# Kernel optimization log

Measured on AMD Instinct MI355X. Metric: run time of the kernel, lower is better.

## Reference

```python
import jax, jax.numpy as jnp
import numpy as np

NPOINT, RADIUS, NSAMPLE = 1024, 0.2, 32


def setup_inputs() -> dict:
    key = jax.random.key(0)
    ks = jax.random.split(key, 8)
    B, N, C = 16, 4096, 64
    xyz = jax.random.uniform(ks[0], (B, N, 3), jnp.float32)          # points in unit cube
    features = jax.random.normal(ks[1], (B, N, C), jnp.float32)
    W1 = jax.random.normal(ks[2], (64, C + 3), jnp.float32) * 0.05   # Conv2d(67,64,1)
    b1 = jnp.zeros((64,), jnp.float32)
    W2 = jax.random.normal(ks[3], (64, 64), jnp.float32) * 0.05      # Conv2d(64,64,1)
    b2 = jnp.zeros((64,), jnp.float32)
    W3 = jax.random.normal(ks[4], (128, 64), jnp.float32) * 0.05     # Conv2d(64,128,1)
    b3 = jnp.zeros((128,), jnp.float32)
    return {"xyz": xyz, "features": features, "W1": W1, "b1": b1,
            "W2": W2, "b2": b2, "W3": W3, "b3": b3}


def farthest_point_sampling(xyz, npoint):
    # Sequential iterative selection (classic FPS) via lax.scan.
    B, N, _ = xyz.shape
    def step(carry, _):
        dist, far = carry                                            # [B,N], [B]
        centroid = jnp.take_along_axis(xyz, far[:, None, None], axis=1)  # [B,1,3]
        d = jnp.sum((xyz - centroid) ** 2, axis=-1)                  # [B,N]
        dist = jnp.minimum(dist, d)
        nxt = jnp.argmax(dist, axis=-1).astype(jnp.int32)
        return (dist, nxt), far
    init = (jnp.full((B, N), 1e10, xyz.dtype), jnp.zeros((B,), jnp.int32))
    _, idx = jax.lax.scan(step, init, None, length=npoint)
    return idx.T                                                     # [B, npoint]


def ball_query(xyz, new_xyz, radius, nsample):
    B, N, _ = xyz.shape
    S = new_xyz.shape[1]
    sqd = jnp.sum((new_xyz[:, :, None, :] - xyz[:, None, :, :]) ** 2, axis=-1)  # [B,S,N]
    idx = jnp.broadcast_to(jnp.arange(N, dtype=jnp.int32), (B, S, N))
    idx = jnp.where(sqd > radius * radius, N, idx)
    idx = jnp.sort(idx, axis=-1)[:, :, :nsample]                     # first nsample in-ball
    first = idx[:, :, :1]
    return jnp.where(idx == N, first, idx)                           # pad with first hit


def _gather(points, idx):
    # points [B,N,C], idx [B,S,K] -> [B,S,K,C]
    B = points.shape[0]
    return points[jnp.arange(B)[:, None, None], idx]


def reference(xyz, features, W1, b1, W2, b2, W3, b3):
    fps_idx = farthest_point_sampling(xyz, NPOINT)                   # [B,S]
    new_xyz = jnp.take_along_axis(xyz, fps_idx[..., None], axis=1)   # [B,S,3]
    idx = ball_query(xyz, new_xyz, RADIUS, NSAMPLE)                  # [B,S,K]
    grouped_xyz = _gather(xyz, idx) - new_xyz[:, :, None, :]         # [B,S,K,3]
    grouped = jnp.concatenate([grouped_xyz, _gather(features, idx)], axis=-1)  # [B,S,K,3+C]
    x = jnp.transpose(grouped, (0, 3, 2, 1))                          # [B, 3+C, K, S]
    # 1x1 Conv2d stack (no activations in the original Sequential)
    x = jnp.einsum('oc,bckn->bokn', W1, x) + b1[None, :, None, None]
    x = jnp.einsum('oc,bckn->bokn', W2, x) + b2[None, :, None, None]
    x = jnp.einsum('oc,bckn->bokn', W3, x) + b3[None, :, None, None]
    new_features = jnp.max(x, axis=2)                                 # max over nsample -> [B,128,S]
    return new_xyz, new_features, fps_idx
```

## Files before the change

kernel.cpp:

```cpp
#include <hip/hip_runtime.h>
#include <cstdint>
#include <cstddef>

#define B_      16
#define N_      4096
#define CFEAT_  64
#define NPOINT_ 1024
#define NSAMPLE_ 32
#define CIN_    67
#define KPAD_   96
#define COUT_   128
#define R2_     0.04f

typedef float f32x2 __attribute__((ext_vector_type(2)));
typedef float f32x4 __attribute__((ext_vector_type(4)));
typedef short bf16x8 __attribute__((ext_vector_type(8)));

__device__ __forceinline__ f32x2 pk_sub(f32x2 a, f32x2 b) {
  f32x2 d;
  asm("v_pk_add_f32 %0, %1, %2 neg_lo:[0,1] neg_hi:[0,1]" : "=v"(d) : "v"(a), "v"(b));
  return d;
}
__device__ __forceinline__ f32x2 pk_mul(f32x2 a, f32x2 b) {
  f32x2 d;
  asm("v_pk_mul_f32 %0, %1, %2" : "=v"(d) : "v"(a), "v"(b));
  return d;
}
__device__ __forceinline__ f32x2 pk_add(f32x2 a, f32x2 b) {
  f32x2 d;
  asm("v_pk_add_f32 %0, %1, %2" : "=v"(d) : "v"(a), "v"(b));
  return d;
}
__device__ __forceinline__ float max3f(float a, float b, float c) {
  float r;
  asm("v_max3_f32 %0, %1, %2, %3" : "=v"(r) : "v"(a), "v"(b), "v"(c));
  return r;
}
__device__ __forceinline__ unsigned short f2bf(float f) {
  uint32_t u = __float_as_uint(f);
  uint32_t r = (u + 0x7FFFu + ((u >> 16) & 1u)) >> 16;
  return (unsigned short)r;
}

template<int CTRL>
__device__ __forceinline__ float dpp_fmax(float v) {
  int s = __builtin_amdgcn_update_dpp(__float_as_int(v), __float_as_int(v),
                                      CTRL, 0xF, 0xF, false);
  return fmaxf(v, __int_as_float(s));
}

__global__ __launch_bounds__(256) void k_fuse(
    const float* __restrict__ W1, const float* __restrict__ b1,
    const float* __restrict__ W2, const float* __restrict__ b2,
    const float* __restrict__ W3, const float* __restrict__ b3,
    unsigned short* __restrict__ Wbf ,
    float* __restrict__ beff ) {
  __shared__ float W21[64][CIN_];
  __shared__ float b21[64];
  int t = threadIdx.x;
  for (int i = t; i < 64 * CIN_; i += 256) {
    int o = i / CIN_, c = i - o * CIN_;
    float s = 0.f;
    for (int j = 0; j < 64; ++j) s = fmaf(W2[o * 64 + j], W1[j * CIN_ + c], s);
    W21[o][c] = s;
  }
  if (t < 64) {
    float s = b2[t];
    for (int j = 0; j < 64; ++j) s = fmaf(W2[t * 64 + j], b1[j], s);
    b21[t] = s;
  }
  __syncthreads();
  for (int i = t; i < COUT_ * (KPAD_ / 2); i += 256) {
    int o = i / (KPAD_ / 2), cp = i - o * (KPAD_ / 2);
    int c0 = 2 * cp, c1 = c0 + 1;
    float s0 = 0.f, s1 = 0.f;
    if (c0 < CIN_) {
      float a = 0.f;
      for (int j = 0; j < 64; ++j) a = fmaf(W3[o * 64 + j], W21[j][c0], a);
      s0 = a;
    }
    if (c1 < CIN_) {
      float a = 0.f;
      for (int j = 0; j < 64; ++j) a = fmaf(W3[o * 64 + j], W21[j][c1], a);
      s1 = a;
    }
    uint32_t pk = (uint32_t)f2bf(s0) | ((uint32_t)f2bf(s1) << 16);
    ((uint32_t*)Wbf)[o * (KPAD_ / 2) + cp] = pk;
  }
  if (t < COUT_) {
    float s = b3[t];
    for (int j = 0; j < 64; ++j) s = fmaf(W3[t * 64 + j], b21[j], s);
    beff[t] = s;
  }
}

__global__ __launch_bounds__(256) void k_fps(
    const float* __restrict__ xyz,
    float* __restrict__ out_newxyz, float* __restrict__ out_fpsf) {
  int b = blockIdx.x, t = threadIdx.x;
  const float* X = xyz + (size_t)b * (N_ * 3);
  __shared__ __align__(16) float Xsh[N_ * 3];
  __shared__ __align__(16) float4 res[NPOINT_];
  __shared__ __align__(16) float4 redA[2][4];
  __shared__ __align__(16) int    redI[2][4];
  for (int i = t; i < (N_ * 3) / 4; i += 256)
    ((float4*)Xsh)[i] = ((const float4*)X)[i];
  __syncthreads();

  const int base = t * 16;
  f32x2 px[8], py[8], pz[8], dist[8];
#pragma unroll
  for (int k = 0; k < 8; ++k) {
    int j = base + 2 * k;
    px[k] = f32x2{Xsh[j * 3 + 0], Xsh[j * 3 + 3]};
    py[k] = f32x2{Xsh[j * 3 + 1], Xsh[j * 3 + 4]};
    pz[k] = f32x2{Xsh[j * 3 + 2], Xsh[j * 3 + 5]};
    dist[k] = f32x2{1e10f, 1e10f};
  }
  float cx = Xsh[0], cy = Xsh[1], cz = Xsh[2];
  if (t == 0) res[0] = make_float4(cx, cy, cz, 0.f);
  const int w = t >> 6, lane = t & 63;

  for (int it = 1; it < NPOINT_; ++it) {
    f32x2 cxx = {cx, cx}, cyy = {cy, cy}, czz = {cz, cz};
    {
#pragma clang fp contract(off)
#pragma unroll
      for (int k = 0; k < 8; ++k) {
        f32x2 dx = pk_sub(px[k], cxx);
        f32x2 dy = pk_sub(py[k], cyy);
        f32x2 dz = pk_sub(pz[k], czz);
        f32x2 s = pk_add(pk_add(pk_mul(dx, dx), pk_mul(dy, dy)), pk_mul(dz, dz));
        dist[k].x = fminf(dist[k].x, s.x);
        dist[k].y = fminf(dist[k].y, s.y);
      }
    }
    float m0 = max3f(dist[0].x, dist[0].y, dist[1].x);
    float m1 = max3f(dist[1].y, dist[2].x, dist[2].y);
    float m2 = max3f(dist[3].x, dist[3].y, dist[4].x);
    float m3 = max3f(dist[4].y, dist[5].x, dist[5].y);
    float m4 = max3f(dist[6].x, dist[6].y, dist[7].x);
    float n0 = max3f(m0, m1, m2);
    float n1 = max3f(m3, m4, dist[7].y);
    float bv = fmaxf(n0, n1);

    int jm = 15;
#pragma unroll
    for (int j = 14; j >= 0; --j) {
      float dj = (j & 1) ? dist[j >> 1].y : dist[j >> 1].x;
      jm = (dj == bv) ? j : jm;
    }
    int bi = base + jm;

    float v = bv;
    v = dpp_fmax<0xB1>(v);
    v = dpp_fmax<0x4E>(v);
    v = dpp_fmax<0x141>(v);
    v = dpp_fmax<0x140>(v);
    v = dpp_fmax<0x142>(v);
    v = dpp_fmax<0x143>(v);
    float wmax = __int_as_float(__builtin_amdgcn_readlane(__float_as_int(v), 63));
    unsigned long long msk = __ballot(bv == wmax);
    int winlane = __ffsll((long long)msk) - 1;
    int wbi = __builtin_amdgcn_readlane(bi, winlane);

    int par = it & 1;
    if (lane == 0) {
      float x = Xsh[wbi * 3 + 0], y = Xsh[wbi * 3 + 1], z = Xsh[wbi * 3 + 2];
      redA[par][w] = make_float4(wmax, x, y, z);
      redI[par][w] = wbi;
    }
    __syncthreads();
    float4 a0 = redA[par][0], a1 = redA[par][1];
    float4 a2 = redA[par][2], a3 = redA[par][3];
    int4 ii = *(const int4*)&redI[par][0];
    bool g01 = a1.x > a0.x, g23 = a3.x > a2.x;
    float4 s01 = g01 ? a1 : a0; int i01 = g01 ? ii.y : ii.x;
    float4 s23 = g23 ? a3 : a2; int i23 = g23 ? ii.w : ii.z;
    bool g = s23.x > s01.x;
    float4 s = g ? s23 : s01; int wi = g ? i23 : i01;
    cx = s.y; cy = s.z; cz = s.w;
    if (t == 0) res[it] = make_float4(cx, cy, cz, (float)wi);
  }
  __syncthreads();
  float* nx = out_newxyz + (size_t)b * (NPOINT_ * 3);
  float* nf = out_fpsf + (size_t)b * NPOINT_;
  for (int i = t; i < NPOINT_; i += 256) {
    float4 r = res[i];
    nx[i * 3 + 0] = r.x; nx[i * 3 + 1] = r.y; nx[i * 3 + 2] = r.z;
    nf[i] = r.w;
  }
}

__global__ __launch_bounds__(256) void k_group(
    const float* __restrict__ xyz, const float* __restrict__ feat,
    const float* __restrict__ newxyz,
    const unsigned short* __restrict__ Wbf, const float* __restrict__ beff,
    float* __restrict__ outF) {
  __shared__ __align__(16) unsigned short Wl[COUT_ * KPAD_];
  __shared__ __align__(16) unsigned short gl[128 * KPAD_];
  __shared__ int   idxs[128];
  __shared__ float ctr[4][3];
  __shared__ float bsh[COUT_];
  __shared__ __align__(16) float outsh[4][COUT_];
  int t = threadIdx.x;
  int b = blockIdx.y;
  int sbase = blockIdx.x * 4;
  int w = t >> 6, lane = t & 63;

  for (int i = t; i < (COUT_ * KPAD_ * 2) / 16; i += 256)
    ((float4*)Wl)[i] = ((const float4*)Wbf)[i];
  if (t < COUT_) bsh[t] = beff[t];

  {
#pragma clang fp contract(off)
    const float* X = xyz + (size_t)b * (N_ * 3);
    int s = b * NPOINT_ + sbase + w;
    float cx = newxyz[(size_t)s * 3 + 0];
    float cy = newxyz[(size_t)s * 3 + 1];
    float cz = newxyz[(size_t)s * 3 + 2];
    if (lane == 0) { ctr[w][0] = cx; ctr[w][1] = cy; ctr[w][2] = cz; }
    int total = 0, first = 0;
    for (int j = 0; j < N_ / 64; ++j) {
      if (total >= NSAMPLE_) break;
      int p = j * 64 + lane;
      float dx = X[p * 3 + 0] - cx, dy = X[p * 3 + 1] - cy, dz = X[p * 3 + 2] - cz;
      float t0 = dx * dx, t1 = dy * dy, t2 = dz * dz;
      float d = (t0 + t1) + t2;
      bool inb = !(d > R2_);
      unsigned long long mask = __ballot(inb);
      if (total == 0 && mask) first = j * 64 + (__ffsll((long long)mask) - 1);
      if (inb) {
        int slot = total + __popcll(mask & ((1ull << lane) - 1ull));
        if (slot < NSAMPLE_) idxs[w * NSAMPLE_ + slot] = p;
      }
      total += (int)__popcll(mask);
    }
    for (int slot = total + lane; slot < NSAMPLE_; slot += 64)
      idxs[w * NSAMPLE_ + slot] = first;
  }
  __syncthreads();

  for (int i = t; i < 128 * (KPAD_ / 2); i += 256) {
    int n = i / (KPAD_ / 2), cp = i - n * (KPAD_ / 2);
    int p = idxs[n];
    const float* Xp = xyz + ((size_t)b * N_ + p) * 3;
    const float* Fp = feat + ((size_t)b * N_ + p) * CFEAT_;
    float v0 = 0.f, v1 = 0.f;
    if (cp == 0)      { v0 = Xp[0] - ctr[n >> 5][0]; v1 = Xp[1] - ctr[n >> 5][1]; }
    else if (cp == 1) { v0 = Xp[2] - ctr[n >> 5][2]; v1 = Fp[0]; }
    else if (cp <= 32){ v0 = Fp[2 * cp - 3]; v1 = Fp[2 * cp - 2]; }
    else if (cp == 33){ v0 = Fp[63]; }
    uint32_t pk = (uint32_t)f2bf(v0) | ((uint32_t)f2bf(v1) << 16);
    *(uint32_t*)((char*)gl + n * (KPAD_ * 2) + cp * 4) = pk;
  }
  __syncthreads();

  int q = lane >> 4, c16 = lane & 15;
  f32x4 acc[2][8];
#pragma unroll
  for (int tm = 0; tm < 2; ++tm)
#pragma unroll
    for (int tn = 0; tn < 8; ++tn)
#pragma unroll
      for (int j = 0; j < 4; ++j) acc[tm][tn][j] = 0.f;

  const char* Wb = (const char*)Wl;
  const char* Gb = (const char*)gl;
#pragma unroll
  for (int ks = 0; ks < 3; ++ks) {
    int cb = q * 16 + ks * 64;
    bf16x8 a0 = *(const bf16x8*)(Wb + (32 * w + c16) * (KPAD_ * 2) + cb);
    bf16x8 a1 = *(const bf16x8*)(Wb + (32 * w + 16 + c16) * (KPAD_ * 2) + cb);
#pragma unroll
    for (int tn = 0; tn < 8; ++tn) {
      bf16x8 bb = *(const bf16x8*)(Gb + (16 * tn + c16) * (KPAD_ * 2) + cb);
      acc[0][tn] = __builtin_amdgcn_mfma_f32_16x16x32_bf16(a0, bb, acc[0][tn], 0, 0, 0);
      acc[1][tn] = __builtin_amdgcn_mfma_f32_16x16x32_bf16(a1, bb, acc[1][tn], 0, 0, 0);
    }
  }

#pragma unroll
  for (int tm = 0; tm < 2; ++tm) {
#pragma unroll
    for (int si = 0; si < 4; ++si) {
      f32x4 mx;
#pragma unroll
      for (int j = 0; j < 4; ++j)
        mx[j] = fmaxf(acc[tm][2 * si][j], acc[tm][2 * si + 1][j]);
#pragma unroll
      for (int off = 1; off <= 8; off <<= 1) {
#pragma unroll
        for (int j = 0; j < 4; ++j) mx[j] = fmaxf(mx[j], __shfl_xor(mx[j], off));
      }
      if (c16 == 0)
        *(f32x4*)&outsh[si][32 * w + 16 * tm + 4 * q] = mx;
    }
  }
  __syncthreads();
  if (t < COUT_) {
    float bb2 = bsh[t];
    float4 v = make_float4(outsh[0][t] + bb2, outsh[1][t] + bb2,
                           outsh[2][t] + bb2, outsh[3][t] + bb2);
    *(float4*)&outF[((size_t)b * COUT_ + t) * NPOINT_ + sbase] = v;
  }
}

extern "C" void kernel_launch(void* const* d_in, const int* in_sizes, int n_in,
                              void* d_out, int out_size, void* d_ws, size_t ws_size,
                              hipStream_t stream) {
  (void)in_sizes; (void)n_in; (void)out_size; (void)ws_size;
  const float* xyz  = (const float*)d_in[0];
  const float* feat = (const float*)d_in[1];
  const float* W1 = (const float*)d_in[2];
  const float* b1 = (const float*)d_in[3];
  const float* W2 = (const float*)d_in[4];
  const float* b2 = (const float*)d_in[5];
  const float* W3 = (const float*)d_in[6];
  const float* b3 = (const float*)d_in[7];

  float* out = (float*)d_out;
  float* out_newxyz = out;
  float* out_feat   = out + (size_t)B_ * NPOINT_ * 3;
  float* out_fpsf   = out_feat + (size_t)B_ * COUT_ * NPOINT_;

  char* ws = (char*)d_ws;
  unsigned short* Wbf = (unsigned short*)ws;
  float* beff = (float*)(ws + (size_t)COUT_ * KPAD_ * 2);

  k_fuse<<<1, 256, 0, stream>>>(W1, b1, W2, b2, W3, b3, Wbf, beff);
  k_fps<<<B_, 256, 0, stream>>>(xyz, out_newxyz, out_fpsf);
  k_group<<<dim3(NPOINT_ / 4, B_), 256, 0, stream>>>(xyz, feat, out_newxyz, Wbf, beff, out_feat);
}
```

Before: 932.9 us.

## Transpose xyz to SoA, prefetch ball query, vectorize feature gather with reordered channels

Adds a prep kernel that transposes xyz into per-batch SoA arrays, which the ball query reads coalesced, one tile ahead of use. The grouped-feature build now loads each neighbor's features as float4 into the first 64 channels. The xyz offsets move to channels 64-66, and the fused weight columns are permuted in k_fuse to match. This costs an extra kernel launch, an xyzT buffer in workspace and a zero-fill of the shared tile.

```diff
diff --git a/kernel.cpp b/kernel.cpp
--- a/kernel.cpp
+++ b/kernel.cpp
@@ -47,6 +47,17 @@
   int s = __builtin_amdgcn_update_dpp(__float_as_int(v), __float_as_int(v),
                                       CTRL, 0xF, 0xF, false);
   return fmaxf(v, __int_as_float(s));
+}
+
+__global__ __launch_bounds__(256) void k_prep(
+    const float* __restrict__ xyz, float* __restrict__ xyzT) {
+  int gp = blockIdx.x * 256 + threadIdx.x;
+  int b = gp >> 12, p = gp & (N_ - 1);
+  float x = xyz[(size_t)gp * 3 + 0];
+  float y = xyz[(size_t)gp * 3 + 1];
+  float z = xyz[(size_t)gp * 3 + 2];
+  float* T = xyzT + (size_t)b * 3 * N_;
+  T[p] = x; T[N_ + p] = y; T[2 * N_ + p] = z;
 }
 
 __global__ __launch_bounds__(256) void k_fuse(
@@ -73,15 +84,17 @@
   for (int i = t; i < COUT_ * (KPAD_ / 2); i += 256) {
     int o = i / (KPAD_ / 2), cp = i - o * (KPAD_ / 2);
     int c0 = 2 * cp, c1 = c0 + 1;
+    int s0i = (c0 < 64) ? c0 + 3 : ((c0 < 67) ? c0 - 64 : -1);
+    int s1i = (c1 < 64) ? c1 + 3 : ((c1 < 67) ? c1 - 64 : -1);
     float s0 = 0.f, s1 = 0.f;
-    if (c0 < CIN_) {
+    if (s0i >= 0) {
       float a = 0.f;
-      for (int j = 0; j < 64; ++j) a = fmaf(W3[o * 64 + j], W21[j][c0], a);
+      for (int j = 0; j < 64; ++j) a = fmaf(W3[o * 64 + j], W21[j][s0i], a);
       s0 = a;
     }
-    if (c1 < CIN_) {
+    if (s1i >= 0) {
       float a = 0.f;
-      for (int j = 0; j < 64; ++j) a = fmaf(W3[o * 64 + j], W21[j][c1], a);
+      for (int j = 0; j < 64; ++j) a = fmaf(W3[o * 64 + j], W21[j][s1i], a);
       s1 = a;
     }
     uint32_t pk = (uint32_t)f2bf(s0) | ((uint32_t)f2bf(s1) << 16);
@@ -193,7 +206,7 @@
 }
 
 __global__ __launch_bounds__(256) void k_group(
-    const float* __restrict__ xyz, const float* __restrict__ feat,
+    const float* __restrict__ xyzT, const float* __restrict__ feat,
     const float* __restrict__ newxyz,
     const unsigned short* __restrict__ Wbf, const float* __restrict__ beff,
     float* __restrict__ outF) {
@@ -210,21 +223,32 @@
 
   for (int i = t; i < (COUT_ * KPAD_ * 2) / 16; i += 256)
     ((float4*)Wl)[i] = ((const float4*)Wbf)[i];
+  for (int i = t; i < (128 * KPAD_ * 2) / 16; i += 256)
+    ((float4*)gl)[i] = make_float4(0.f, 0.f, 0.f, 0.f);
   if (t < COUT_) bsh[t] = beff[t];
+
+  const float* Xx = xyzT + (size_t)b * 3 * N_;
+  const float* Xy = Xx + N_;
+  const float* Xz = Xx + 2 * N_;
 
   {
 #pragma clang fp contract(off)
-    const float* X = xyz + (size_t)b * (N_ * 3);
     int s = b * NPOINT_ + sbase + w;
     float cx = newxyz[(size_t)s * 3 + 0];
     float cy = newxyz[(size_t)s * 3 + 1];
     float cz = newxyz[(size_t)s * 3 + 2];
     if (lane == 0) { ctr[w][0] = cx; ctr[w][1] = cy; ctr[w][2] = cz; }
     int total = 0, first = 0;
-    for (int j = 0; j < N_ / 64; ++j) {
-      if (total >= NSAMPLE_) break;
-      int p = j * 64 + lane;
-      float dx = X[p * 3 + 0] - cx, dy = X[p * 3 + 1] - cy, dz = X[p * 3 + 2] - cz;
+    float xx = Xx[lane], yy = Xy[lane], zz = Xz[lane];
+    int j = 0;
+    while (true) {
+      int jn = j + 1;
+      float nx2 = 0.f, ny2 = 0.f, nz2 = 0.f;
+      if (jn < N_ / 64) {
+        int pn = jn * 64 + lane;
+        nx2 = Xx[pn]; ny2 = Xy[pn]; nz2 = Xz[pn];
+      }
+      float dx = xx - cx, dy = yy - cy, dz = zz - cz;
       float t0 = dx * dx, t1 = dy * dy, t2 = dz * dz;
       float d = (t0 + t1) + t2;
       bool inb = !(d > R2_);
@@ -232,27 +256,33 @@
       if (total == 0 && mask) first = j * 64 + (__ffsll((long long)mask) - 1);
       if (inb) {
         int slot = total + __popcll(mask & ((1ull << lane) - 1ull));
-        if (slot < NSAMPLE_) idxs[w * NSAMPLE_ + slot] = p;
+        if (slot < NSAMPLE_) idxs[w * NSAMPLE_ + slot] = j * 64 + lane;
       }
       total += (int)__popcll(mask);
+      if (total >= NSAMPLE_ || jn >= N_ / 64) break;
+      xx = nx2; yy = ny2; zz = nz2; j = jn;
     }
     for (int slot = total + lane; slot < NSAMPLE_; slot += 64)
       idxs[w * NSAMPLE_ + slot] = first;
   }
   __syncthreads();
 
-  for (int i = t; i < 128 * (KPAD_ / 2); i += 256) {
-    int n = i / (KPAD_ / 2), cp = i - n * (KPAD_ / 2);
+  for (int i = t; i < 128 * 16; i += 256) {
+    int n = i >> 4, cg = i & 15;
     int p = idxs[n];
-    const float* Xp = xyz + ((size_t)b * N_ + p) * 3;
-    const float* Fp = feat + ((size_t)b * N_ + p) * CFEAT_;
-    float v0 = 0.f, v1 = 0.f;
-    if (cp == 0)      { v0 = Xp[0] - ctr[n >> 5][0]; v1 = Xp[1] - ctr[n >> 5][1]; }
-    else if (cp == 1) { v0 = Xp[2] - ctr[n >> 5][2]; v1 = Fp[0]; }
-    else if (cp <= 32){ v0 = Fp[2 * cp - 3]; v1 = Fp[2 * cp - 2]; }
-    else if (cp == 33){ v0 = Fp[63]; }
-    uint32_t pk = (uint32_t)f2bf(v0) | ((uint32_t)f2bf(v1) << 16);
-    *(uint32_t*)((char*)gl + n * (KPAD_ * 2) + cp * 4) = pk;
+    float4 f = *(const float4*)(feat + (((size_t)b * N_ + p) * CFEAT_) + 4 * cg);
+    uint32_t lo = (uint32_t)f2bf(f.x) | ((uint32_t)f2bf(f.y) << 16);
+    uint32_t hi = (uint32_t)f2bf(f.z) | ((uint32_t)f2bf(f.w) << 16);
+    *(uint2*)((char*)gl + n * (KPAD_ * 2) + cg * 8) = make_uint2(lo, hi);
+  }
+  if (t < 128) {
+    int n = t, p = idxs[n];
+    float x = Xx[p] - ctr[n >> 5][0];
+    float y = Xy[p] - ctr[n >> 5][1];
+    float z = Xz[p] - ctr[n >> 5][2];
+    uint32_t lo = (uint32_t)f2bf(x) | ((uint32_t)f2bf(y) << 16);
+    uint32_t hi = (uint32_t)f2bf(z);
+    *(uint2*)((char*)gl + n * (KPAD_ * 2) + 128) = make_uint2(lo, hi);
   }
   __syncthreads();
 
@@ -327,8 +357,10 @@
   char* ws = (char*)d_ws;
   unsigned short* Wbf = (unsigned short*)ws;
   float* beff = (float*)(ws + (size_t)COUT_ * KPAD_ * 2);
-
+  float* xyzT = beff + COUT_;
+
+  k_prep<<<(B_ * N_) / 256, 256, 0, stream>>>(xyz, xyzT);
   k_fuse<<<1, 256, 0, stream>>>(W1, b1, W2, b2, W3, b3, Wbf, beff);
   k_fps<<<B_, 256, 0, stream>>>(xyz, out_newxyz, out_fpsf);
-  k_group<<<dim3(NPOINT_ / 4, B_), 256, 0, stream>>>(xyz, feat, out_newxyz, Wbf, beff, out_feat);
-}
+  k_group<<<dim3(NPOINT_ / 4, B_), 256, 0, stream>>>(xyzT, feat, out_newxyz, Wbf, beff, out_feat);
+}
```

Result: faster. 854.1 us (-8.4%).
